# Kernel tuning notes

Measured on AMD Instinct MI355X. Metric: run time of the kernel, lower is better.

The kernel has to match this reference:

```python
import jax, jax.numpy as jnp
import numpy as np

N, E, F, C, H, L, ED = 100000, 1600000, 128, 16, 2, 2, 4
EPS = 1e-5
NEG_SLOPE = 0.2


def setup_inputs() -> dict:
    key = jax.random.key(0)
    ks = jax.random.split(key, 32)
    s = 0.1
    inp = {
        "x": jax.random.normal(ks[0], (N, F), dtype=jnp.float32),
        "edge_index": jax.random.randint(ks[1], (2, E), 0, N, dtype=jnp.int64),
        "edge_attr": jax.random.uniform(ks[2], (E, ED), dtype=jnp.float32),
        "embed_W": jax.random.normal(ks[3], (F, C)) * s,
        "embed_b": jnp.zeros((C,), jnp.float32),
        "ln0_w": jnp.ones((C,), jnp.float32),
        "ln0_b": jnp.zeros((C,), jnp.float32),
        "Wl": jax.random.normal(ks[4], (L, C, H * C)) * s,
        "bl": jnp.zeros((L, H * C), jnp.float32),
        "Wr": jax.random.normal(ks[5], (L, C, H * C)) * s,
        "br": jnp.zeros((L, H * C), jnp.float32),
        "We": jax.random.normal(ks[6], (L, ED, H * C)) * s,
        "att": jax.random.normal(ks[7], (L, H, C)) * s,
        "gat_b": jnp.zeros((L, H * C), jnp.float32),
        "n1_w": jnp.ones((L, H * C), jnp.float32),
        "n1_b": jnp.zeros((L, H * C), jnp.float32),
        "lin_W": jax.random.normal(ks[8], (L, H * C, C)) * s,
        "lin_b": jnp.zeros((L, C), jnp.float32),
        "n2_w": jnp.ones((L, C), jnp.float32),
        "n2_b": jnp.zeros((L, C), jnp.float32),
    }
    return inp


def _node_ln(v, w, b):
    # torch.nn.LayerNorm over the feature dim (per node)
    mu = v.mean(-1, keepdims=True)
    var = ((v - mu) ** 2).mean(-1, keepdims=True)
    return (v - mu) / jnp.sqrt(var + EPS) * w + b


def _graph_ln(v, w, b):
    # PyG norm.LayerNorm(mode='graph'): normalize over ALL nodes and channels
    mu = v.mean()
    vc = v - mu
    return vc / jnp.sqrt((vc * vc).mean() + EPS) * w + b


def reference(x, edge_index, edge_attr, embed_W, embed_b, ln0_w, ln0_b,
              Wl, bl, Wr, br, We, att, gat_b, n1_w, n1_b,
              lin_W, lin_b, n2_w, n2_b):
    n = x.shape[0]
    heads, c = att.shape[1], att.shape[2]
    layers = Wl.shape[0]

    # node embedding MLP (dropout = identity in eval)
    h = jax.nn.relu(_node_ln(x @ embed_W + embed_b, ln0_w, ln0_b))

    # add self-loops (fill_value=0.0 -> zero edge features, lin_edge has no bias)
    loop = jnp.arange(n)
    src = jnp.concatenate([edge_index[0], loop])
    dst = jnp.concatenate([edge_index[1], loop])

    hs = [h]
    for i in range(layers):
        xl = (h @ Wl[i] + bl[i]).reshape(n, heads, c)   # source transform (x_j)
        xr = (h @ Wr[i] + br[i]).reshape(n, heads, c)   # target transform (x_i)
        ew = (edge_attr @ We[i]).reshape(-1, heads, c)
        ew = jnp.concatenate([ew, jnp.zeros((n, heads, c), ew.dtype)], axis=0)

        msg = xl[src] + xr[dst] + ew                      # [E+N, H, C]
        logits = jnp.einsum('ehc,hc->eh', jax.nn.leaky_relu(msg, NEG_SLOPE), att[i])
        m = jax.ops.segment_max(logits, dst, num_segments=n)
        ex = jnp.exp(logits - m[dst])
        den = jax.ops.segment_sum(ex, dst, num_segments=n)
        alpha = ex / den[dst]                             # segment softmax over dst

        g = jax.ops.segment_sum(alpha[..., None] * xl[src], dst, num_segments=n)
        g = g.reshape(n, heads * c) + gat_b[i]

        g = jax.nn.relu(_graph_ln(g, n1_w[i], n1_b[i]))
        g = g @ lin_W[i] + lin_b[i]
        g = _graph_ln(g, n2_w[i], n2_b[i])
        h = jax.nn.relu(g + h)                            # residual + relu
        hs.append(h)

    # JumpingKnowledge mode='max': elementwise max over layer outputs
    return jnp.max(jnp.stack(hs, axis=0), axis=0)
```

## Files before the change

### kernel.cpp

```cpp
#include <hip/hip_runtime.h>

#define N_NODES 100000
#define N_EDGES 1600000
#define NF 128
#define NC 16
#define NH 2
#define HC 32
#define NL 2
#define NED 4
#define EPS 1e-5f
#define NEG 0.2f
#define NBUCK 196
#define P1_CHUNK 4096
#define P1_BLKS ((N_EDGES + P1_CHUNK - 1) / P1_CHUNK)
#define AGG_BLKS ((N_NODES + 15) / 16)
#define MID_BLKS ((N_NODES + 15) / 16)

typedef __attribute__((ext_vector_type(2))) float f32x2;

__device__ __forceinline__ unsigned short f2bf(float f) {
    unsigned int u = __float_as_uint(f);
    u += 0x7fffu + ((u >> 16) & 1u);
    return (unsigned short)(u >> 16);
}
__device__ __forceinline__ float bf2f(unsigned short u) {
    return __uint_as_float(((unsigned int)u) << 16);
}
__device__ __forceinline__ unsigned int pack_bf2(float a, float b) {
    return (unsigned int)f2bf(a) | ((unsigned int)f2bf(b) << 16);
}
__device__ __forceinline__ float bflo(int u) {
    return __uint_as_float(((unsigned int)u) << 16);
}
__device__ __forceinline__ float bfhi(int u) {
    return __uint_as_float(((unsigned int)u) & 0xffff0000u);
}
__device__ __forceinline__ f32x2 sp2(float v) { f32x2 r; r.x = v; r.y = v; return r; }
__device__ __forceinline__ f32x2 bf2_gather(const unsigned short* base, unsigned boff) {
    unsigned u = *(const unsigned*)((const char*)base + boff);
    f32x2 r;
    r.x = __uint_as_float(u << 16);
    r.y = __uint_as_float(u & 0xffff0000u);
    return r;
}

__global__ __launch_bounds__(256) void k_embed(
    const float* __restrict__ x, const float* __restrict__ W,
    const float* __restrict__ b, const float* __restrict__ lnw,
    const float* __restrict__ lnb, float* __restrict__ h, float* __restrict__ jk)
{
    __shared__ __align__(16) float WsT[NC][NF + 4];
    __shared__ __align__(16) float xs[16][NF + 4];
    const int t = threadIdx.x;
    for (int i = t; i < NF * NC; i += 256) {
        int f = i >> 4, c = i & 15;
        WsT[c][f] = W[i];
    }
    const int n0 = blockIdx.x * 16;
    const float4* x4 = (const float4*)x;
    for (int i = t; i < 16 * (NF / 4); i += 256) {
        int r = i >> 5, f4 = i & 31;
        int n = n0 + r;
        float4 v = (n < N_NODES) ? x4[(size_t)n * (NF / 4) + f4]
                                 : make_float4(0.f, 0.f, 0.f, 0.f);
        *(float4*)&xs[r][f4 * 4] = v;
    }
    __syncthreads();
    const int r = t >> 4;
    const int c = t & 15;
    const int n = n0 + r;
    float acc = b[c];
#pragma unroll
    for (int f4 = 0; f4 < NF / 4; ++f4) {
        float4 xv = *(const float4*)&xs[r][f4 * 4];
        float4 wv = *(const float4*)&WsT[c][f4 * 4];
        acc += xv.x * wv.x + xv.y * wv.y + xv.z * wv.z + xv.w * wv.w;
    }
    float s = acc;
    for (int m = 8; m >= 1; m >>= 1) s += __shfl_xor(s, m, 16);
    float mu = s * (1.f / 16.f);
    float d = acc - mu;
    float v = d * d;
    for (int m = 8; m >= 1; m >>= 1) v += __shfl_xor(v, m, 16);
    float inv = rsqrtf(v * (1.f / 16.f) + EPS);
    float out = fmaxf(d * inv * lnw[c] + lnb[c], 0.f);
    if (n < N_NODES) {
        h[(size_t)n * NC + c]  = out;
        jk[(size_t)n * NC + c] = out;
    }
}

__global__ __launch_bounds__(256) void k_bhist(
    const int* __restrict__ dst, int* __restrict__ bcnt)
{
    __shared__ int hist[256];
    const int t = threadIdx.x;
    hist[t] = 0;
    __syncthreads();
    const int e0 = blockIdx.x * P1_CHUNK;
    const int cnt = min(P1_CHUNK, N_EDGES - e0);
    for (int i = t; i < cnt; i += 256)
        atomicAdd(&hist[dst[e0 + i] >> 9], 1);
    __syncthreads();
    if (hist[t] > 0) atomicAdd(&bcnt[t], hist[t]);
}

__global__ __launch_bounds__(256) void k_bscan(
    const int* __restrict__ bcnt, int* __restrict__ bbase, int* __restrict__ bcur)
{
    __shared__ int tmp[256];
    const int t = threadIdx.x;
    int v0 = bcnt[t];
    tmp[t] = v0;
    __syncthreads();
    for (int off = 1; off < 256; off <<= 1) {
        int v = (t >= off) ? tmp[t - off] : 0;
        __syncthreads();
        tmp[t] += v;
        __syncthreads();
    }
    int excl = tmp[t] - v0;
    bbase[t] = excl;
    bcur[t]  = excl;
    if (t == 255) bbase[256] = tmp[t];
}

__global__ __launch_bounds__(256) void k_pass1(
    const int* __restrict__ src, const int* __restrict__ dst,
    const float4* __restrict__ ea4, int* __restrict__ bcur,
    int4* __restrict__ tmp_rec)
{
    __shared__ int2 stage[P1_CHUNK];
    __shared__ unsigned char bstage[P1_CHUNK];
    __shared__ int hist[256];
    __shared__ int exc[256];
    __shared__ int gbase[256];
    __shared__ int scanbuf[256];
    const int t = threadIdx.x;
    const int e0 = blockIdx.x * P1_CHUNK;
    const int cnt = min(P1_CHUNK, N_EDGES - e0);
    hist[t] = 0;
    __syncthreads();
    int mys[16], myb[16], myp[16];
    int nv = 0;
#pragma unroll
    for (int k = 0; k < 16; ++k) {
        int i = k * 256 + t;
        if (i < cnt) {
            int e = e0 + i;
            int d = dst[e];
            mys[nv] = src[e];
            myb[nv] = d >> 9;
            myp[nv] = (e << 9) | (d & 511);
            atomicAdd(&hist[d >> 9], 1);
            ++nv;
        }
    }
    __syncthreads();
    int hv = hist[t];
    scanbuf[t] = hv;
    __syncthreads();
    for (int off = 1; off < 256; off <<= 1) {
        int v = (t >= off) ? scanbuf[t - off] : 0;
        __syncthreads();
        scanbuf[t] += v;
        __syncthreads();
    }
    int ex = scanbuf[t] - hv;
    hist[t] = ex;
    exc[t]  = ex;
    __syncthreads();
    for (int k = 0; k < nv; ++k) {
        int pos = atomicAdd(&hist[myb[k]], 1);
        stage[pos]  = make_int2(mys[k], myp[k]);
        bstage[pos] = (unsigned char)myb[k];
    }
    __syncthreads();
    {
        int c = hist[t] - exc[t];
        gbase[t] = (c > 0) ? atomicAdd(&bcur[t], c) : 0;
    }
    __syncthreads();
    for (int i = t; i < cnt; i += 256) {
        int b = bstage[i];
        int2 se = stage[i];
        int e  = (int)(((unsigned int)se.y) >> 9);
        int dl = se.y & 511;
        float4 ea = ea4[e];
        int gpos = gbase[b] + (i - exc[b]);
        tmp_rec[gpos] = make_int4(se.x, dl,
                                  (int)pack_bf2(ea.x, ea.y),
                                  (int)pack_bf2(ea.z, ea.w));
    }
}

__global__ __launch_bounds__(256) void k_pass2(
    const int* __restrict__ bbase, const int4* __restrict__ tmp_rec,
    int* __restrict__ offsets, int4* __restrict__ csr)
{
    __shared__ int hist[512];
    __shared__ int cur[512];
    __shared__ int scanbuf[256];
    const int b = blockIdx.x, t = threadIdx.x;
    const int ebeg = bbase[b], eend = bbase[b + 1];
    hist[t] = 0; hist[t + 256] = 0;
    __syncthreads();
    for (int i = ebeg + t; i < eend; i += 256)
        atomicAdd(&hist[tmp_rec[i].y], 1);
    __syncthreads();
    int a0 = hist[2 * t], a1 = hist[2 * t + 1];
    int pair = a0 + a1;
    scanbuf[t] = pair;
    __syncthreads();
    for (int off = 1; off < 256; off <<= 1) {
        int v = (t >= off) ? scanbuf[t - off] : 0;
        __syncthreads();
        scanbuf[t] += v;
        __syncthreads();
    }
    int ex2 = scanbuf[t] - pair;
    cur[2 * t]     = ex2;
    cur[2 * t + 1] = ex2 + a0;
    __syncthreads();
    const int n0 = b * 512;
#pragma unroll
    for (int k = 0; k < 2; ++k) {
        int i = t + k * 256;
        int n = n0 + i;
        if (n < N_NODES) offsets[n] = ebeg + cur[i];
    }
    if (b == NBUCK - 1 && t == 0) offsets[N_NODES] = N_EDGES;
    __syncthreads();
    for (int i = ebeg + t; i < eend; i += 256) {
        int4 rec = tmp_rec[i];
        int pos = ebeg + atomicAdd(&cur[rec.y], 1);
        csr[pos] = rec;
    }
}

__global__ __launch_bounds__(256) void k_trans(
    const float* __restrict__ h, const float* __restrict__ Wl, const float* __restrict__ bl,
    const float* __restrict__ Wr, const float* __restrict__ br,
    unsigned short* __restrict__ xl, unsigned short* __restrict__ xr)
{
    __shared__ float Wls[NC * HC], Wrs[NC * HC];
    __shared__ float hs[8][NC + 1];
    const int t = threadIdx.x;
    for (int i = t; i < NC * HC; i += 256) { Wls[i] = Wl[i]; Wrs[i] = Wr[i]; }
    const int n0 = blockIdx.x * 8;
    for (int i = t; i < 8 * NC; i += 256) {
        int r = i >> 4, c = i & 15;
        int n = n0 + r;
        hs[r][c] = (n < N_NODES) ? h[(size_t)n * NC + c] : 0.f;
    }
    __syncthreads();
    const int r = t >> 5;
    const int j = t & 31;
    const int n = n0 + r;
    float al = bl[j], ar = br[j];
#pragma unroll
    for (int c = 0; c < NC; ++c) {
        float hv = hs[r][c];
        al += hv * Wls[c * HC + j];
        ar += hv * Wrs[c * HC + j];
    }
    if (n < N_NODES) {
        xl[(size_t)n * HC + j] = f2bf(al);
        xr[(size_t)n * HC + j] = f2bf(ar);
    }
}

__device__ __forceinline__ float hsum8(float p) {
    p += __shfl_xor(p, 1, 8);
    p += __shfl_xor(p, 2, 8);
    p += __shfl_xor(p, 4, 8);
    return p;
}

__global__ __launch_bounds__(256) void k_agg(
    const int* __restrict__ offsets, const int4* __restrict__ csr,
    const float* __restrict__ We, const float* __restrict__ att,
    const float* __restrict__ gat_b,
    const unsigned short* __restrict__ xl, const unsigned short* __restrict__ xr,
    float* __restrict__ g, float2* __restrict__ part)
{
    __shared__ float Wes[NED * HC];
    __shared__ float atts[HC], gbs[HC];
    const int t = threadIdx.x;
    if (t < NED * HC) Wes[t] = We[t];
    if (t < HC) { atts[t] = att[t]; gbs[t] = gat_b[t]; }
    __syncthreads();
    const int grp = t >> 4;
    const int j2  = t & 15;
    const int d = blockIdx.x * 16 + grp;
    f32x2 gv = sp2(0.f);
    if (d < N_NODES) {
        f32x2 aj; aj.x = atts[2 * j2]; aj.y = atts[2 * j2 + 1];
        f32x2 w0; w0.x = Wes[2 * j2];          w0.y = Wes[2 * j2 + 1];
        f32x2 w1; w1.x = Wes[HC + 2 * j2];     w1.y = Wes[HC + 2 * j2 + 1];
        f32x2 w2; w2.x = Wes[2 * HC + 2 * j2]; w2.y = Wes[2 * HC + 2 * j2 + 1];
        f32x2 w3; w3.x = Wes[3 * HC + 2 * j2]; w3.y = Wes[3 * HC + 2 * j2 + 1];
        const unsigned jb = (unsigned)(j2 << 2);
        const f32x2 xld = bf2_gather(xl, ((unsigned)d << 6) + jb);
        const f32x2 xrd = bf2_gather(xr, ((unsigned)d << 6) + jb);
        f32x2 m = xld + xrd;
        m.x = fmaxf(m.x, NEG * m.x);
        m.y = fmaxf(m.y, NEG * m.y);
        float eh = __expf(hsum8(m.x * aj.x + m.y * aj.y));
        f32x2 acc = sp2(eh) * xld;
        float den = eh;
        const int base = offsets[d];
        const int deg  = offsets[d + 1] - base;
        int k = 0;
        for (; k + 4 <= deg; k += 4) {
            const int b0 = base + k;
            const int4 r0 = csr[b0],     r1 = csr[b0 + 1];
            const int4 r2 = csr[b0 + 2], r3 = csr[b0 + 3];
            const f32x2 x0 = bf2_gather(xl, ((unsigned)r0.x << 6) + jb);
            const f32x2 x1 = bf2_gather(xl, ((unsigned)r1.x << 6) + jb);
            const f32x2 x2 = bf2_gather(xl, ((unsigned)r2.x << 6) + jb);
            const f32x2 x3 = bf2_gather(xl, ((unsigned)r3.x << 6) + jb);
            f32x2 m0 = x0 + xrd, m1 = x1 + xrd, m2 = x2 + xrd, m3 = x3 + xrd;
            m0 += sp2(bflo(r0.z)) * w0; m1 += sp2(bflo(r1.z)) * w0;
            m2 += sp2(bflo(r2.z)) * w0; m3 += sp2(bflo(r3.z)) * w0;
            m0 += sp2(bfhi(r0.z)) * w1; m1 += sp2(bfhi(r1.z)) * w1;
            m2 += sp2(bfhi(r2.z)) * w1; m3 += sp2(bfhi(r3.z)) * w1;
            m0 += sp2(bflo(r0.w)) * w2; m1 += sp2(bflo(r1.w)) * w2;
            m2 += sp2(bflo(r2.w)) * w2; m3 += sp2(bflo(r3.w)) * w2;
            m0 += sp2(bfhi(r0.w)) * w3; m1 += sp2(bfhi(r1.w)) * w3;
            m2 += sp2(bfhi(r2.w)) * w3; m3 += sp2(bfhi(r3.w)) * w3;
            m0.x = fmaxf(m0.x, NEG * m0.x); m0.y = fmaxf(m0.y, NEG * m0.y);
            m1.x = fmaxf(m1.x, NEG * m1.x); m1.y = fmaxf(m1.y, NEG * m1.y);
            m2.x = fmaxf(m2.x, NEG * m2.x); m2.y = fmaxf(m2.y, NEG * m2.y);
            m3.x = fmaxf(m3.x, NEG * m3.x); m3.y = fmaxf(m3.y, NEG * m3.y);
            float p0 = m0.x * aj.x + m0.y * aj.y;
            float p1 = m1.x * aj.x + m1.y * aj.y;
            float p2 = m2.x * aj.x + m2.y * aj.y;
            float p3 = m3.x * aj.x + m3.y * aj.y;
            p0 += __shfl_xor(p0, 1, 8); p1 += __shfl_xor(p1, 1, 8);
            p2 += __shfl_xor(p2, 1, 8); p3 += __shfl_xor(p3, 1, 8);
            p0 += __shfl_xor(p0, 2, 8); p1 += __shfl_xor(p1, 2, 8);
            p2 += __shfl_xor(p2, 2, 8); p3 += __shfl_xor(p3, 2, 8);
            p0 += __shfl_xor(p0, 4, 8); p1 += __shfl_xor(p1, 4, 8);
            p2 += __shfl_xor(p2, 4, 8); p3 += __shfl_xor(p3, 4, 8);
            const float ee0 = __expf(p0), ee1 = __expf(p1);
            const float ee2 = __expf(p2), ee3 = __expf(p3);
            acc += sp2(ee0) * x0; acc += sp2(ee1) * x1;
            acc += sp2(ee2) * x2; acc += sp2(ee3) * x3;
            den += ee0 + ee1 + ee2 + ee3;
        }
        for (; k < deg; ++k) {
            const int4 r = csr[base + k];
            const f32x2 xv = bf2_gather(xl, ((unsigned)r.x << 6) + jb);
            f32x2 mm = xv + xrd;
            mm += sp2(bflo(r.z)) * w0; mm += sp2(bfhi(r.z)) * w1;
            mm += sp2(bflo(r.w)) * w2; mm += sp2(bfhi(r.w)) * w3;
            mm.x = fmaxf(mm.x, NEG * mm.x); mm.y = fmaxf(mm.y, NEG * mm.y);
            const float ee = __expf(hsum8(mm.x * aj.x + mm.y * aj.y));
            acc += sp2(ee) * xv;
            den += ee;
        }
        const float invd = 1.f / den;
        gv.x = acc.x * invd + gbs[2 * j2];
        gv.y = acc.y * invd + gbs[2 * j2 + 1];
        *(float2*)&g[(size_t)d * HC + 2 * j2] = make_float2(gv.x, gv.y);
    }
    float s = gv.x + gv.y, ss = gv.x * gv.x + gv.y * gv.y;
    for (int m = 32; m >= 1; m >>= 1) { s += __shfl_xor(s, m); ss += __shfl_xor(ss, m); }
    __shared__ float sr[4], ssr[4];
    const int w = t >> 6;
    if ((t & 63) == 0) { sr[w] = s; ssr[w] = ss; }
    __syncthreads();
    if (t == 0) part[blockIdx.x] = make_float2(sr[0] + sr[1] + sr[2] + sr[3],
                                               ssr[0] + ssr[1] + ssr[2] + ssr[3]);
}

__global__ __launch_bounds__(256) void k_red(
    const float2* __restrict__ part, int n, double* __restrict__ out)
{
    const int t = threadIdx.x;
    double s = 0.0, ss = 0.0;
    for (int i = t; i < n; i += 256) {
        float2 p = part[i];
        s += (double)p.x; ss += (double)p.y;
    }
    for (int m = 32; m >= 1; m >>= 1) { s += __shfl_xor(s, m); ss += __shfl_xor(ss, m); }
    __shared__ double sr[4], ssr[4];
    const int w = t >> 6;
    if ((t & 63) == 0) { sr[w] = s; ssr[w] = ss; }
    __syncthreads();
    if (t == 0) {
        out[0] = sr[0] + sr[1] + sr[2] + sr[3];
        out[1] = ssr[0] + ssr[1] + ssr[2] + ssr[3];
    }
}

__global__ __launch_bounds__(256) void k_mid(
    const float* __restrict__ g,
    const float* __restrict__ n1w, const float* __restrict__ n1b,
    const float* __restrict__ linW, const float* __restrict__ linb,
    const double* __restrict__ stats1, float* __restrict__ g2,
    float2* __restrict__ part)
{
    __shared__ float Ws[HC * NC];
    __shared__ float rs[16][HC + 1];
    const int t = threadIdx.x;
    for (int i = t; i < HC * NC; i += 256) Ws[i] = linW[i];
    const double cnt = (double)N_NODES * HC;
    const double mud = stats1[0] / cnt;
    const float mu  = (float)mud;
    const float var = (float)(stats1[1] / cnt - mud * mud);
    const float inv = rsqrtf(var + EPS);
    const int n0 = blockIdx.x * 16;
    for (int i = t; i < 16 * HC; i += 256) {
        int r = i >> 5, j = i & 31;
        int n = n0 + r;
        float v = (n < N_NODES) ? g[(size_t)n * HC + j] : mu;
        v = (v - mu) * inv * n1w[j] + n1b[j];
        rs[r][j] = fmaxf(v, 0.f);
    }
    __syncthreads();
    const int r = t >> 4, c = t & 15;
    const int n = n0 + r;
    float acc = linb[c];
#pragma unroll
    for (int j = 0; j < HC; ++j) acc += rs[r][j] * Ws[j * NC + c];
    float val = (n < N_NODES) ? acc : 0.f;
    if (n < N_NODES) g2[(size_t)n * NC + c] = acc;
    float s = val, ss = val * val;
    for (int m = 32; m >= 1; m >>= 1) { s += __shfl_xor(s, m); ss += __shfl_xor(ss, m); }
    __shared__ float sr[4], ssr[4];
    const int w = t >> 6;
    if ((t & 63) == 0) { sr[w] = s; ssr[w] = ss; }
    __syncthreads();
    if (t == 0) part[blockIdx.x] = make_float2(sr[0] + sr[1] + sr[2] + sr[3],
                                               ssr[0] + ssr[1] + ssr[2] + ssr[3]);
}

__global__ __launch_bounds__(256) void k_ftrans(
    const float* __restrict__ g2, const float* __restrict__ n2w,
    const float* __restrict__ n2b, const double* __restrict__ stats2,
    float* __restrict__ h, float* __restrict__ jk,
    const float* __restrict__ Wl, const float* __restrict__ bl,
    const float* __restrict__ Wr, const float* __restrict__ br,
    unsigned short* __restrict__ xl, unsigned short* __restrict__ xr)
{
    __shared__ float Wls[NC * HC], Wrs[NC * HC];
    __shared__ float hs[8][NC + 1];
    const int t = threadIdx.x;
    for (int i = t; i < NC * HC; i += 256) { Wls[i] = Wl[i]; Wrs[i] = Wr[i]; }
    const double cnt = (double)N_NODES * NC;
    const double mud = stats2[0] / cnt;
    const float mu  = (float)mud;
    const float var = (float)(stats2[1] / cnt - mud * mud);
    const float inv = rsqrtf(var + EPS);
    const int n0 = blockIdx.x * 8;
    if (t < 8 * NC) {
        int r = t >> 4, c = t & 15;
        int n = n0 + r;
        if (n < N_NODES) {
            size_t idx = (size_t)n * NC + c;
            float v = (g2[idx] - mu) * inv * n2w[c] + n2b[c];
            float hn = fmaxf(v + h[idx], 0.f);
            h[idx] = hn;
            jk[idx] = fmaxf(jk[idx], hn);
            hs[r][c] = hn;
        } else hs[r][c] = 0.f;
    }
    __syncthreads();
    const int r = t >> 5;
    const int j = t & 31;
    const int n = n0 + r;
    float al = bl[j], ar = br[j];
#pragma unroll
    for (int c = 0; c < NC; ++c) {
        float hv = hs[r][c];
        al += hv * Wls[c * HC + j];
        ar += hv * Wrs[c * HC + j];
    }
    if (n < N_NODES) {
        xl[(size_t)n * HC + j] = f2bf(al);
        xr[(size_t)n * HC + j] = f2bf(ar);
    }
}

__global__ __launch_bounds__(256) void k_final(
    const float* __restrict__ g2, const float* __restrict__ n2w,
    const float* __restrict__ n2b, const double* __restrict__ stats2,
    float* __restrict__ h, float* __restrict__ jk)
{
    const int i = blockIdx.x * 256 + threadIdx.x;
    if (i >= N_NODES * NC) return;
    const double cnt = (double)N_NODES * NC;
    const double mud = stats2[0] / cnt;
    const float mu  = (float)mud;
    const float var = (float)(stats2[1] / cnt - mud * mud);
    const float inv = rsqrtf(var + EPS);
    const int c = i & (NC - 1);
    float v = (g2[i] - mu) * inv * n2w[c] + n2b[c];
    float hn = fmaxf(v + h[i], 0.f);
    h[i] = hn;
    jk[i] = fmaxf(jk[i], hn);
}

extern "C" void kernel_launch(void* const* d_in, const int* in_sizes, int n_in,
                              void* d_out, int out_size, void* d_ws, size_t ws_size,
                              hipStream_t stream)
{
    const float* x     = (const float*)d_in[0];
    const int*   eidx  = (const int*)d_in[1];
    const float* eattr = (const float*)d_in[2];
    const float* embW  = (const float*)d_in[3];
    const float* embB  = (const float*)d_in[4];
    const float* ln0w  = (const float*)d_in[5];
    const float* ln0b  = (const float*)d_in[6];
    const float* Wl    = (const float*)d_in[7];
    const float* bl    = (const float*)d_in[8];
    const float* Wr    = (const float*)d_in[9];
    const float* br    = (const float*)d_in[10];
    const float* We    = (const float*)d_in[11];
    const float* att   = (const float*)d_in[12];
    const float* gatb  = (const float*)d_in[13];
    const float* n1w   = (const float*)d_in[14];
    const float* n1b   = (const float*)d_in[15];
    const float* linW  = (const float*)d_in[16];
    const float* linb  = (const float*)d_in[17];
    const float* n2w   = (const float*)d_in[18];
    const float* n2b   = (const float*)d_in[19];
    float* out = (float*)d_out;

    char* ws = (char*)d_ws;
    double* stats = (double*)ws;
    char* p = ws + 1024;
    int* bcnt = (int*)p; p += 1024;
    int* bbase = (int*)p; p += 4096;
    int* bcur  = (int*)p; p += 1024;
    int* offsets = (int*)p; p += (size_t)(N_NODES + 64) * 4;
    float* g = (float*)p; p += (size_t)N_NODES * HC * 4;
    int4* csr = (int4*)p; p += (size_t)N_EDGES * 16;
    int4* tmp_rec = (int4*)p;
    char* q = p;
    p += (size_t)N_EDGES * 16;
    float* hq = (float*)q; q += (size_t)N_NODES * NC * 4;
    unsigned short* xlq = (unsigned short*)q; q += (size_t)N_NODES * HC * 2;
    unsigned short* xrq = (unsigned short*)q; q += (size_t)N_NODES * HC * 2;
    float* g2q = (float*)q;
    float2* part1 = (float2*)p; p += (size_t)AGG_BLKS * 8;
    float2* part2 = (float2*)p; p += (size_t)MID_BLKS * 8;

    const int* srcp = eidx;
    const int* dstp = eidx + N_EDGES;

    hipMemsetAsync(bcnt, 0, 1024, stream);
    k_bhist<<<P1_BLKS, 256, 0, stream>>>(dstp, bcnt);
    k_bscan<<<1, 256, 0, stream>>>(bcnt, bbase, bcur);
    k_pass1<<<P1_BLKS, 256, 0, stream>>>(srcp, dstp, (const float4*)eattr,
                                         bcur, tmp_rec);
    k_pass2<<<NBUCK, 256, 0, stream>>>(bbase, tmp_rec, offsets, csr);

    k_embed<<<(N_NODES + 15) / 16, 256, 0, stream>>>(x, embW, embB, ln0w, ln0b, hq, out);

    k_trans<<<(N_NODES + 7) / 8, 256, 0, stream>>>(hq, Wl, bl, Wr, br, xlq, xrq);
    k_agg<<<AGG_BLKS, 256, 0, stream>>>(
        offsets, csr, We, att, gatb, xlq, xrq, g, part1);
    k_red<<<1, 256, 0, stream>>>(part1, AGG_BLKS, stats);
    k_mid<<<MID_BLKS, 256, 0, stream>>>(
        g, n1w, n1b, linW, linb, stats, g2q, part2);
    k_red<<<1, 256, 0, stream>>>(part2, MID_BLKS, stats + 2);
    k_ftrans<<<(N_NODES + 7) / 8, 256, 0, stream>>>(
        g2q, n2w, n2b, stats + 2, hq, out,
        Wl + NC * HC, bl + HC, Wr + NC * HC, br + HC, xlq, xrq);
    k_agg<<<AGG_BLKS, 256, 0, stream>>>(
        offsets, csr, We + NED * HC, att + HC, gatb + HC, xlq, xrq, g, part1);
    k_red<<<1, 256, 0, stream>>>(part1, AGG_BLKS, stats);
    k_mid<<<MID_BLKS, 256, 0, stream>>>(
        g, n1w + HC, n1b + HC, linW + HC * NC, linb + NC, stats, g2q, part2);
    k_red<<<1, 256, 0, stream>>>(part2, MID_BLKS, stats + 2);
    k_final<<<(N_NODES * NC + 255) / 256, 256, 0, stream>>>(
        g2q, n2w + NC, n2b + NC, stats + 2, hq, out);
}
```

Before: 421.9 us.

## Build CSR via global degree count, scan and atomic scatter

Replaces the two-pass bucketed sort (bucket histogram, bucket scan, local staging pass, per-bucket sort) with a direct CSR build. It now runs a global atomic degree count per destination, a two-level exclusive scan into offsets, then scatters each edge record to its slot using a global atomic cursor. This drops the temporary record buffer and one full read/write pass over the 16-byte records. In exchange it relies on random global atomics and uncoalesced scattered writes, and the order of edges within each node's list becomes nondeterministic.

```diff
diff --git a/kernel.cpp b/kernel.cpp
--- a/kernel.cpp
+++ b/kernel.cpp
@@ -10,9 +10,9 @@
 #define NED 4
 #define EPS 1e-5f
 #define NEG 0.2f
-#define NBUCK 196
-#define P1_CHUNK 4096
-#define P1_BLKS ((N_EDGES + P1_CHUNK - 1) / P1_CHUNK)
+#define SCAN_BLKS 391
+#define DEG_PAD (SCAN_BLKS * 256)
+#define EK_BLKS ((N_EDGES + 1023) / 1024)
 #define AGG_BLKS ((N_NODES + 15) / 16)
 #define MID_BLKS ((N_NODES + 15) / 16)
 
@@ -90,151 +90,99 @@
     }
 }
 
-__global__ __launch_bounds__(256) void k_bhist(
-    const int* __restrict__ dst, int* __restrict__ bcnt)
-{
-    __shared__ int hist[256];
-    const int t = threadIdx.x;
-    hist[t] = 0;
-    __syncthreads();
-    const int e0 = blockIdx.x * P1_CHUNK;
-    const int cnt = min(P1_CHUNK, N_EDGES - e0);
-    for (int i = t; i < cnt; i += 256)
-        atomicAdd(&hist[dst[e0 + i] >> 9], 1);
-    __syncthreads();
-    if (hist[t] > 0) atomicAdd(&bcnt[t], hist[t]);
-}
-
-__global__ __launch_bounds__(256) void k_bscan(
-    const int* __restrict__ bcnt, int* __restrict__ bbase, int* __restrict__ bcur)
-{
-    __shared__ int tmp[256];
-    const int t = threadIdx.x;
-    int v0 = bcnt[t];
-    tmp[t] = v0;
+__global__ __launch_bounds__(256) void k_deg(
+    const int* __restrict__ dst, int* __restrict__ deg)
+{
+    const int t = threadIdx.x;
+    const int e0 = blockIdx.x * 1024;
+#pragma unroll
+    for (int k = 0; k < 4; ++k) {
+        int e = e0 + k * 256 + t;
+        if (e < N_EDGES) atomicAdd(&deg[dst[e]], 1);
+    }
+}
+
+__global__ __launch_bounds__(256) void k_lscan(
+    const int* __restrict__ deg, int* __restrict__ cur, int* __restrict__ bsum)
+{
+    __shared__ int buf[256];
+    const int t = threadIdx.x;
+    const int n = blockIdx.x * 256 + t;
+    int v = deg[n];
+    buf[t] = v;
     __syncthreads();
     for (int off = 1; off < 256; off <<= 1) {
-        int v = (t >= off) ? tmp[t - off] : 0;
+        int x = (t >= off) ? buf[t - off] : 0;
         __syncthreads();
-        tmp[t] += v;
+        buf[t] += x;
         __syncthreads();
     }
-    int excl = tmp[t] - v0;
-    bbase[t] = excl;
-    bcur[t]  = excl;
-    if (t == 255) bbase[256] = tmp[t];
-}
-
-__global__ __launch_bounds__(256) void k_pass1(
+    cur[n] = buf[t] - v;
+    if (t == 255) bsum[blockIdx.x] = buf[255];
+}
+
+__global__ __launch_bounds__(256) void k_sscan(
+    const int* __restrict__ bsum, int* __restrict__ bpref)
+{
+    __shared__ int a[256];
+    const int t = threadIdx.x;
+    int v0 = bsum[t];
+    a[t] = v0;
+    __syncthreads();
+    for (int off = 1; off < 256; off <<= 1) {
+        int x = (t >= off) ? a[t - off] : 0;
+        __syncthreads();
+        a[t] += x;
+        __syncthreads();
+    }
+    int exclA = a[t] - v0;
+    int totalA = a[255];
+    __syncthreads();
+    int v1 = (256 + t < SCAN_BLKS) ? bsum[256 + t] : 0;
+    a[t] = v1;
+    __syncthreads();
+    for (int off = 1; off < 256; off <<= 1) {
+        int x = (t >= off) ? a[t - off] : 0;
+        __syncthreads();
+        a[t] += x;
+        __syncthreads();
+    }
+    int exclB = a[t] - v1;
+    bpref[t] = exclA;
+    if (256 + t < SCAN_BLKS) bpref[256 + t] = totalA + exclB;
+}
+
+__global__ __launch_bounds__(256) void k_oadd(
+    const int* __restrict__ bpref, int* __restrict__ cur,
+    int* __restrict__ offsets)
+{
+    const int t = threadIdx.x;
+    const int b = blockIdx.x;
+    const int n = b * 256 + t;
+    int v = bpref[b] + cur[n];
+    if (n < N_NODES) { offsets[n] = v; cur[n] = v; }
+    if (b == SCAN_BLKS - 1 && t == 0) offsets[N_NODES] = N_EDGES;
+}
+
+__global__ __launch_bounds__(256) void k_scatter(
     const int* __restrict__ src, const int* __restrict__ dst,
-    const float4* __restrict__ ea4, int* __restrict__ bcur,
-    int4* __restrict__ tmp_rec)
-{
-    __shared__ int2 stage[P1_CHUNK];
-    __shared__ unsigned char bstage[P1_CHUNK];
-    __shared__ int hist[256];
-    __shared__ int exc[256];
-    __shared__ int gbase[256];
-    __shared__ int scanbuf[256];
-    const int t = threadIdx.x;
-    const int e0 = blockIdx.x * P1_CHUNK;
-    const int cnt = min(P1_CHUNK, N_EDGES - e0);
-    hist[t] = 0;
-    __syncthreads();
-    int mys[16], myb[16], myp[16];
-    int nv = 0;
+    const float4* __restrict__ ea4, int* __restrict__ cur,
+    int4* __restrict__ csr)
+{
+    const int t = threadIdx.x;
+    const int e0 = blockIdx.x * 1024;
 #pragma unroll
-    for (int k = 0; k < 16; ++k) {
-        int i = k * 256 + t;
-        if (i < cnt) {
-            int e = e0 + i;
+    for (int k = 0; k < 4; ++k) {
+        int e = e0 + k * 256 + t;
+        if (e < N_EDGES) {
             int d = dst[e];
-            mys[nv] = src[e];
-            myb[nv] = d >> 9;
-            myp[nv] = (e << 9) | (d & 511);
-            atomicAdd(&hist[d >> 9], 1);
-            ++nv;
+            int s = src[e];
+            float4 ea = ea4[e];
+            int pos = atomicAdd(&cur[d], 1);
+            csr[pos] = make_int4(s, 0,
+                                 (int)pack_bf2(ea.x, ea.y),
+                                 (int)pack_bf2(ea.z, ea.w));
         }
-    }
-    __syncthreads();
-    int hv = hist[t];
-    scanbuf[t] = hv;
-    __syncthreads();
-    for (int off = 1; off < 256; off <<= 1) {
-        int v = (t >= off) ? scanbuf[t - off] : 0;
-        __syncthreads();
-        scanbuf[t] += v;
-        __syncthreads();
-    }
-    int ex = scanbuf[t] - hv;
-    hist[t] = ex;
-    exc[t]  = ex;
-    __syncthreads();
-    for (int k = 0; k < nv; ++k) {
-        int pos = atomicAdd(&hist[myb[k]], 1);
-        stage[pos]  = make_int2(mys[k], myp[k]);
-        bstage[pos] = (unsigned char)myb[k];
-    }
-    __syncthreads();
-    {
-        int c = hist[t] - exc[t];
-        gbase[t] = (c > 0) ? atomicAdd(&bcur[t], c) : 0;
-    }
-    __syncthreads();
-    for (int i = t; i < cnt; i += 256) {
-        int b = bstage[i];
-        int2 se = stage[i];
-        int e  = (int)(((unsigned int)se.y) >> 9);
-        int dl = se.y & 511;
-        float4 ea = ea4[e];
-        int gpos = gbase[b] + (i - exc[b]);
-        tmp_rec[gpos] = make_int4(se.x, dl,
-                                  (int)pack_bf2(ea.x, ea.y),
-                                  (int)pack_bf2(ea.z, ea.w));
-    }
-}
-
-__global__ __launch_bounds__(256) void k_pass2(
-    const int* __restrict__ bbase, const int4* __restrict__ tmp_rec,
-    int* __restrict__ offsets, int4* __restrict__ csr)
-{
-    __shared__ int hist[512];
-    __shared__ int cur[512];
-    __shared__ int scanbuf[256];
-    const int b = blockIdx.x, t = threadIdx.x;
-    const int ebeg = bbase[b], eend = bbase[b + 1];
-    hist[t] = 0; hist[t + 256] = 0;
-    __syncthreads();
-    for (int i = ebeg + t; i < eend; i += 256)
-        atomicAdd(&hist[tmp_rec[i].y], 1);
-    __syncthreads();
-    int a0 = hist[2 * t], a1 = hist[2 * t + 1];
-    int pair = a0 + a1;
-    scanbuf[t] = pair;
-    __syncthreads();
-    for (int off = 1; off < 256; off <<= 1) {
-        int v = (t >= off) ? scanbuf[t - off] : 0;
-        __syncthreads();
-        scanbuf[t] += v;
-        __syncthreads();
-    }
-    int ex2 = scanbuf[t] - pair;
-    cur[2 * t]     = ex2;
-    cur[2 * t + 1] = ex2 + a0;
-    __syncthreads();
-    const int n0 = b * 512;
-#pragma unroll
-    for (int k = 0; k < 2; ++k) {
-        int i = t + k * 256;
-        int n = n0 + i;
-        if (n < N_NODES) offsets[n] = ebeg + cur[i];
-    }
-    if (b == NBUCK - 1 && t == 0) offsets[N_NODES] = N_EDGES;
-    __syncthreads();
-    for (int i = ebeg + t; i < eend; i += 256) {
-        int4 rec = tmp_rec[i];
-        int pos = ebeg + atomicAdd(&cur[rec.y], 1);
-        csr[pos] = rec;
     }
 }
 
@@ -532,31 +480,33 @@
     char* ws = (char*)d_ws;
     double* stats = (double*)ws;
     char* p = ws + 1024;
-    int* bcnt = (int*)p; p += 1024;
-    int* bbase = (int*)p; p += 4096;
-    int* bcur  = (int*)p; p += 1024;
+    int* bsum  = (int*)p; p += 2048;
+    int* bpref = (int*)p; p += 2048;
     int* offsets = (int*)p; p += (size_t)(N_NODES + 64) * 4;
     float* g = (float*)p; p += (size_t)N_NODES * HC * 4;
     int4* csr = (int4*)p; p += (size_t)N_EDGES * 16;
-    int4* tmp_rec = (int4*)p;
     char* q = p;
     p += (size_t)N_EDGES * 16;
-    float* hq = (float*)q; q += (size_t)N_NODES * NC * 4;
-    unsigned short* xlq = (unsigned short*)q; q += (size_t)N_NODES * HC * 2;
-    unsigned short* xrq = (unsigned short*)q; q += (size_t)N_NODES * HC * 2;
-    float* g2q = (float*)q;
+    int* deg = (int*)q;
+    int* cur = (int*)(q + (size_t)DEG_PAD * 4 + 1024);
+    float* hq = (float*)q; 
+    char* q2 = q + (size_t)N_NODES * NC * 4;
+    unsigned short* xlq = (unsigned short*)q2; q2 += (size_t)N_NODES * HC * 2;
+    unsigned short* xrq = (unsigned short*)q2; q2 += (size_t)N_NODES * HC * 2;
+    float* g2q = (float*)q2;
     float2* part1 = (float2*)p; p += (size_t)AGG_BLKS * 8;
     float2* part2 = (float2*)p; p += (size_t)MID_BLKS * 8;
 
     const int* srcp = eidx;
     const int* dstp = eidx + N_EDGES;
 
-    hipMemsetAsync(bcnt, 0, 1024, stream);
-    k_bhist<<<P1_BLKS, 256, 0, stream>>>(dstp, bcnt);
-    k_bscan<<<1, 256, 0, stream>>>(bcnt, bbase, bcur);
-    k_pass1<<<P1_BLKS, 256, 0, stream>>>(srcp, dstp, (const float4*)eattr,
-                                         bcur, tmp_rec);
-    k_pass2<<<NBUCK, 256, 0, stream>>>(bbase, tmp_rec, offsets, csr);
+    hipMemsetAsync(deg, 0, (size_t)DEG_PAD * 4, stream);
+    k_deg<<<EK_BLKS, 256, 0, stream>>>(dstp, deg);
+    k_lscan<<<SCAN_BLKS, 256, 0, stream>>>(deg, cur, bsum);
+    k_sscan<<<1, 256, 0, stream>>>(bsum, bpref);
+    k_oadd<<<SCAN_BLKS, 256, 0, stream>>>(bpref, cur, offsets);
+    k_scatter<<<EK_BLKS, 256, 0, stream>>>(srcp, dstp, (const float4*)eattr,
+                                           cur, csr);
 
     k_embed<<<(N_NODES + 15) / 16, 256, 0, stream>>>(x, embW, embB, ln0w, ln0b, hq, out);
 
```

New measurement: 509.1 us. +20.7%, slower.
